# Performance work log

Measured on AMD Instinct MI355X. Metric: run time of the kernel, lower is better.

Reference implementation:

```python
import jax, jax.numpy as jnp
import numpy as np

B, S, HID, H = 1, 2048, 512, 8
D = HID // H            # head_dim = 64
N_TIP, N_FAC = 16, 256
SCALE = 1.0 / np.sqrt(D).astype(np.float32)


def _dominant_dim_indices():
    # dominant_fcs = arange(n_tip) % (head_dim//2), identical for every head
    pair_dim = max(1, D // 2)
    fc = jnp.arange(N_TIP) % pair_dim                      # [n_tip]
    dim_idx = jnp.stack((fc * 2, fc * 2 + 1), axis=-1).reshape(-1)  # [2*n_tip]
    return jnp.clip(dim_idx, 0, D - 1)


def setup_inputs() -> dict:
    key = jax.random.key(0)
    kx, kq, kk, kv, ko = jax.random.split(key, 5)
    s = 1.0 / np.sqrt(HID)
    return {
        "x": jax.random.normal(kx, (B, S, HID), jnp.float32),
        "wq": jax.random.normal(kq, (HID, HID), jnp.float32) * s,
        "wk": jax.random.normal(kk, (HID, HID), jnp.float32) * s,
        "wv": jax.random.normal(kv, (HID, HID), jnp.float32) * s,
        "wo": jax.random.normal(ko, (HID, HID), jnp.float32) * s,
    }


def reference(x, wq, wk, wv, wo):
    # projections (nn.Linear, no bias): y = x @ W.T; split into heads -> [B,H,S,D]
    def split_heads(y):
        return y.reshape(B, S, H, D).transpose(0, 2, 1, 3)

    q = split_heads(x @ wq.T)
    k = split_heads(x @ wk.T)
    v = split_heads(x @ wv.T)

    dim_idx = _dominant_dim_indices()                      # [2*n_tip]
    q_sub = q[..., dim_idx]                                # [B,H,S,2*n_tip]
    k_sub = k[..., dim_idx]
    importance = jnp.einsum("bhqf,bhkf->bhqk", q_sub, k_sub)  # [B,H,S,S]

    n_sel = min(N_FAC, S)
    _, top_idx = jax.lax.top_k(importance, n_sel)          # [B,H,S,n_sel]

    # gather selected K/V per query: [B,H,S,n_sel,D]
    k_sel = jnp.take_along_axis(k[:, :, None], top_idx[..., None], axis=3)
    v_sel = jnp.take_along_axis(v[:, :, None], top_idx[..., None], axis=3)

    scores = jnp.einsum("bhqd,bhqkd->bhqk", q, k_sel) * SCALE
    attn = jax.nn.softmax(scores, axis=-1)
    out = jnp.einsum("bhqk,bhqkd->bhqd", attn, v_sel)      # [B,H,S,D]

    out = out.transpose(0, 2, 1, 3).reshape(B, S, HID)
    return out @ wo.T
```

## Files before the change

### kernel.cpp

```cpp
#include <hip/hip_runtime.h>

#define S_LEN  2048
#define HIDDEN 512
#define NHEAD  8
#define DHEAD  64
#define NSEL   256
#define ROWS_A 8
#define SCALE_ 0.125f

#define WAVE_SYNC() __asm__ volatile("s_waitcnt lgkmcnt(0)" ::: "memory")

__device__ __forceinline__ unsigned mapu(float f) {
  unsigned u = __float_as_uint(f);
  return (u & 0x80000000u) ? ~u : (u | 0x80000000u);
}
__device__ __forceinline__ float unmapu(unsigned x) {
  return __uint_as_float((x & 0x80000000u) ? (x & 0x7FFFFFFFu) : ~x);
}

union H4 { _Float16 h[4]; uint2 u2; };

__device__ __forceinline__ void gemm_nt_body(const float* __restrict__ A,
                                             const float* __restrict__ B,
                                             float* __restrict__ C,
                                             int K, int N, int m0, int n0,
                                             float (*As)[68], float (*Bs)[68]) {
  const int t  = threadIdx.x;
  const int tx = t & 15, ty = t >> 4;
  const int rr = t >> 3, cc = (t & 7) << 2;
  float acc[4][4] = {};

  float4 fa0 = *(const float4*)&A[(size_t)(m0 + rr)      * K + cc];
  float4 fa1 = *(const float4*)&A[(size_t)(m0 + rr + 32) * K + cc];
  float4 fb0 = *(const float4*)&B[(size_t)(n0 + rr)      * K + cc];
  float4 fb1 = *(const float4*)&B[(size_t)(n0 + rr + 32) * K + cc];

  for (int k0 = 0; k0 < K; k0 += 32) {
    __syncthreads();
    As[cc + 0][rr] = fa0.x; As[cc + 1][rr] = fa0.y; As[cc + 2][rr] = fa0.z; As[cc + 3][rr] = fa0.w;
    As[cc + 0][rr + 32] = fa1.x; As[cc + 1][rr + 32] = fa1.y; As[cc + 2][rr + 32] = fa1.z; As[cc + 3][rr + 32] = fa1.w;
    Bs[cc + 0][rr] = fb0.x; Bs[cc + 1][rr] = fb0.y; Bs[cc + 2][rr] = fb0.z; Bs[cc + 3][rr] = fb0.w;
    Bs[cc + 0][rr + 32] = fb1.x; Bs[cc + 1][rr + 32] = fb1.y; Bs[cc + 2][rr + 32] = fb1.z; Bs[cc + 3][rr + 32] = fb1.w;
    __syncthreads();
    if (k0 + 32 < K) {
      fa0 = *(const float4*)&A[(size_t)(m0 + rr)      * K + k0 + 32 + cc];
      fa1 = *(const float4*)&A[(size_t)(m0 + rr + 32) * K + k0 + 32 + cc];
      fb0 = *(const float4*)&B[(size_t)(n0 + rr)      * K + k0 + 32 + cc];
      fb1 = *(const float4*)&B[(size_t)(n0 + rr + 32) * K + k0 + 32 + cc];
    }
#pragma unroll
    for (int kk = 0; kk < 32; ++kk) {
      const float4 a4 = *(const float4*)&As[kk][ty * 4];
      const float4 b4 = *(const float4*)&Bs[kk][tx * 4];
      const float a[4] = {a4.x, a4.y, a4.z, a4.w};
      const float b[4] = {b4.x, b4.y, b4.z, b4.w};
#pragma unroll
      for (int i = 0; i < 4; ++i)
#pragma unroll
        for (int j = 0; j < 4; ++j) acc[i][j] += a[i] * b[j];
    }
  }
#pragma unroll
  for (int i = 0; i < 4; ++i) {
    float4 o = make_float4(acc[i][0], acc[i][1], acc[i][2], acc[i][3]);
    *(float4*)&C[(size_t)(m0 + ty * 4 + i) * N + n0 + tx * 4] = o;
  }
}

__global__ __launch_bounds__(256) void gemm_nt(const float* __restrict__ A,
                                               const float* __restrict__ B,
                                               float* __restrict__ C,
                                               int M, int N, int K) {
  __shared__ float As[32][68];
  __shared__ float Bs[32][68];
  gemm_nt_body(A, B, C, K, N, blockIdx.x * 64, blockIdx.y * 64, As, Bs);
}

__global__ __launch_bounds__(256) void gemm_qkv(const float* __restrict__ x,
                                                const float* __restrict__ wq,
                                                const float* __restrict__ wk,
                                                const float* __restrict__ wv,
                                                float* __restrict__ Qb,
                                                float* __restrict__ Kb,
                                                float* __restrict__ Vb) {
  __shared__ float As[32][68];
  __shared__ float Bs[32][68];
  const int z = blockIdx.z;
  const float* B = (z == 0) ? wq : (z == 1) ? wk : wv;
  float*       C = (z == 0) ? Qb : (z == 1) ? Kb : Vb;
  gemm_nt_body(x, B, C, HIDDEN, HIDDEN, blockIdx.x * 64, blockIdx.y * 64, As, Bs);
}

__global__ __launch_bounds__(256) void score_gemm(const float* __restrict__ Q,
                                                  const float* __restrict__ K,
                                                  unsigned* __restrict__ impu,
                                                  _Float16* __restrict__ sch) {
  __shared__ float Qs[64][132];
  __shared__ float Ks[64][68];
  const int bid  = blockIdx.x;
  const int h    = bid & (NHEAD - 1);
  const int tile = bid >> 3;
  const int q0   = (tile & 15) * 128;
  const int k0   = (tile >> 4) * 64;
  const int t  = threadIdx.x;
  const int tx = t & 15, ty = t >> 4;

#pragma unroll
  for (int s = 0; s < 8; ++s) {
    const int sf = s * 256 + t;
    const int r = sf >> 4, c = (sf & 15) * 4;
    const float4 f = *(const float4*)&Q[(size_t)(q0 + r) * HIDDEN + h * DHEAD + c];
    Qs[c + 0][r] = f.x; Qs[c + 1][r] = f.y; Qs[c + 2][r] = f.z; Qs[c + 3][r] = f.w;
  }
#pragma unroll
  for (int s = 0; s < 4; ++s) {
    const int sf = s * 256 + t;
    const int r = sf >> 4, c = (sf & 15) * 4;
    const float4 f = *(const float4*)&K[(size_t)(k0 + r) * HIDDEN + h * DHEAD + c];
    Ks[c + 0][r] = f.x; Ks[c + 1][r] = f.y; Ks[c + 2][r] = f.z; Ks[c + 3][r] = f.w;
  }
  __syncthreads();

  float acc[8][4] = {};
#pragma unroll
  for (int d = 0; d < 32; ++d) {
    const float4 aa = *(const float4*)&Qs[d][ty * 8];
    const float4 ab = *(const float4*)&Qs[d][ty * 8 + 4];
    const float4 b4 = *(const float4*)&Ks[d][tx * 4];
    const float a[8] = {aa.x, aa.y, aa.z, aa.w, ab.x, ab.y, ab.z, ab.w};
    const float b[4] = {b4.x, b4.y, b4.z, b4.w};
#pragma unroll
    for (int i = 0; i < 8; ++i)
#pragma unroll
      for (int j = 0; j < 4; ++j) acc[i][j] += a[i] * b[j];
  }
  float simp[8][4];
#pragma unroll
  for (int i = 0; i < 8; ++i)
#pragma unroll
    for (int j = 0; j < 4; ++j) simp[i][j] = acc[i][j];
#pragma unroll
  for (int d = 32; d < 64; ++d) {
    const float4 aa = *(const float4*)&Qs[d][ty * 8];
    const float4 ab = *(const float4*)&Qs[d][ty * 8 + 4];
    const float4 b4 = *(const float4*)&Ks[d][tx * 4];
    const float a[8] = {aa.x, aa.y, aa.z, aa.w, ab.x, ab.y, ab.z, ab.w};
    const float b[4] = {b4.x, b4.y, b4.z, b4.w};
#pragma unroll
    for (int i = 0; i < 8; ++i)
#pragma unroll
      for (int j = 0; j < 4; ++j) acc[i][j] += a[i] * b[j];
  }

#pragma unroll
  for (int i = 0; i < 8; ++i) {
    const size_t gr = (size_t)(h * S_LEN) + q0 + ty * 8 + i;
    const size_t off = gr * S_LEN + k0 + tx * 4;
    *(uint4*)&impu[off] = make_uint4(mapu(simp[i][0]), mapu(simp[i][1]),
                                     mapu(simp[i][2]), mapu(simp[i][3]));
    H4 pk;
#pragma unroll
    for (int j = 0; j < 4; ++j) pk.h[j] = (_Float16)(acc[i][j] * SCALE_);
    *(uint2*)&sch[off] = pk.u2;
  }
}

__global__ __launch_bounds__(512) void fused_select_pv(const unsigned* __restrict__ impu,
                                                       const _Float16* __restrict__ sch,
                                                       const float* __restrict__ V,
                                                       float* __restrict__ AO) {
  __shared__ unsigned hist[ROWS_A][256];
  __shared__ float    sbuf[ROWS_A][NSEL];
  __shared__ unsigned ibuf[ROWS_A][NSEL];
  __shared__ unsigned short eqbuf[ROWS_A][64];
  __shared__ unsigned rstate[ROWS_A][2];

  const int t = threadIdx.x, wv = t >> 6, lane = t & 63;
  const unsigned long long lmask = (1ull << lane) - 1ull;
  const size_t gr = (size_t)blockIdx.x * ROWS_A + wv;
  const unsigned* rowp  = impu + gr * S_LEN;
  const _Float16* shrow = sch  + gr * S_LEN;

  uint4 u[8];
  H4    s4[8];
#pragma unroll
  for (int j = 0; j < 8; ++j) {
    u[j]     = *(const uint4*)&rowp[j * 256 + lane * 4];
    s4[j].u2 = *(const uint2*)&shrow[j * 256 + lane * 4];
  }

  unsigned um = u[0].x, uM = u[0].x;
#pragma unroll
  for (int j = 0; j < 8; ++j) {
    um = min(um, min(min(u[j].x, u[j].y), min(u[j].z, u[j].w)));
    uM = max(uM, max(max(u[j].x, u[j].y), max(u[j].z, u[j].w)));
  }
#pragma unroll
  for (int off = 32; off; off >>= 1) {
    um = min(um, (unsigned)__shfl_xor((int)um, off));
    uM = max(uM, (unsigned)__shfl_xor((int)uM, off));
  }

  unsigned bn[8];
  unsigned T;
  if (uM == um) {
    T = uM;
  } else {
    const float vmin  = unmapu(um);
    const float scale = 255.0f / (unmapu(uM) - vmin);

    *(uint4*)&hist[wv][lane * 4] = make_uint4(0u, 0u, 0u, 0u);
    WAVE_SYNC();
#pragma unroll
    for (int j = 0; j < 8; ++j) {
      const unsigned uu[4] = {u[j].x, u[j].y, u[j].z, u[j].w};
      unsigned pk = 0;
#pragma unroll
      for (int e = 0; e < 4; ++e) {
        int bb = (int)((unmapu(uu[e]) - vmin) * scale);
        bb = bb < 0 ? 0 : (bb > 255 ? 255 : bb);
        pk |= (unsigned)bb << (8 * e);
        atomicAdd(&hist[wv][bb], 1u);
      }
      bn[j] = pk;
    }
    WAVE_SYNC();
    {
      const int g = 63 - lane;
      const uint4 c4 = *(const uint4*)&hist[wv][4 * g];
      const unsigned c0 = c4.x, c1 = c4.y, c2 = c4.z, c3 = c4.w;
      const unsigned lsum = c0 + c1 + c2 + c3;
      unsigned incl = lsum;
#pragma unroll
      for (int off = 1; off < 64; off <<= 1) {
        unsigned o = __shfl_up(incl, off);
        if (lane >= off) incl += o;
      }
      const unsigned excl = incl - lsum;
      const unsigned ab3 = excl, ab2 = excl + c3, ab1 = excl + c3 + c2, ab0 = excl + c3 + c2 + c1;
      if (ab3 < NSEL && NSEL <= ab3 + c3) { rstate[wv][0] = 4u*g+3u; rstate[wv][1] = NSEL - ab3; }
      if (ab2 < NSEL && NSEL <= ab2 + c2) { rstate[wv][0] = 4u*g+2u; rstate[wv][1] = NSEL - ab2; }
      if (ab1 < NSEL && NSEL <= ab1 + c1) { rstate[wv][0] = 4u*g+1u; rstate[wv][1] = NSEL - ab1; }
      if (ab0 < NSEL && NSEL <= ab0 + c0) { rstate[wv][0] = 4u*g+0u; rstate[wv][1] = NSEL - ab0; }
    }
    WAVE_SYNC();
    const unsigned B    = rstate[wv][0];
    const unsigned krem = rstate[wv][1];
    const unsigned nb   = hist[wv][B];

    if (nb <= 64) {
      unsigned* ebufu = (unsigned*)&sbuf[wv][0];
      unsigned nbase = 0;
#pragma unroll
      for (int j = 0; j < 8; ++j) {
        const unsigned uu[4] = {u[j].x, u[j].y, u[j].z, u[j].w};
#pragma unroll
        for (int e = 0; e < 4; ++e) {
          const bool inb = (((bn[j] >> (8 * e)) & 0xFFu) == B);
          const unsigned long long m = __ballot(inb);
          if (inb) ebufu[nbase + (unsigned)__popcll(m & lmask)] = uu[e];
          nbase += (unsigned)__popcll(m);
        }
      }
      WAVE_SYNC();
      const unsigned myv = (lane < (int)nb) ? ebufu[lane] : 0u;
      unsigned gtc = 0, eqc = 0;
      for (unsigned jj = 0; jj < nb; ++jj) {
        const unsigned bv = (unsigned)__shfl((int)myv, (int)jj);
        gtc += (bv > myv) ? 1u : 0u;
        eqc += (bv == myv) ? 1u : 0u;
      }
      if (lane < (int)nb && gtc < krem && krem <= gtc + eqc) rstate[wv][0] = myv;
      WAVE_SYNC();
      T = rstate[wv][0];
    } else {
      unsigned m2min = 0xFFFFFFFFu, m2max = 0u;
      for (int i = lane; i < S_LEN; i += 64) {
        const unsigned x = rowp[i];
        int bb = (int)((unmapu(x) - vmin) * scale);
        bb = bb < 0 ? 0 : (bb > 255 ? 255 : bb);
        if (bb == (int)B) { m2min = min(m2min, x); m2max = max(m2max, x); }
      }
#pragma unroll
      for (int off = 32; off; off >>= 1) {
        m2min = min(m2min, (unsigned)__shfl_xor((int)m2min, off));
        m2max = max(m2max, (unsigned)__shfl_xor((int)m2max, off));
      }
      if (m2max == m2min) {
        T = m2max;
      } else {
        const float vlo2   = unmapu(m2min);
        const float scale2 = 255.0f / (unmapu(m2max) - vlo2);
        *(uint4*)&hist[wv][lane * 4] = make_uint4(0u, 0u, 0u, 0u);
        WAVE_SYNC();
        for (int i = lane; i < S_LEN; i += 64) {
          const unsigned x = rowp[i];
          const float v = unmapu(x);
          int bb = (int)((v - vmin) * scale);
          bb = bb < 0 ? 0 : (bb > 255 ? 255 : bb);
          if (bb == (int)B) {
            int b2 = (int)((v - vlo2) * scale2);
            b2 = b2 < 0 ? 0 : (b2 > 255 ? 255 : b2);
            atomicAdd(&hist[wv][b2], 1u);
          }
        }
        WAVE_SYNC();
        {
          const int g = 63 - lane;
          const uint4 c4 = *(const uint4*)&hist[wv][4 * g];
          const unsigned c0 = c4.x, c1 = c4.y, c2 = c4.z, c3 = c4.w;
          const unsigned lsum = c0 + c1 + c2 + c3;
          unsigned incl = lsum;
#pragma unroll
          for (int off = 1; off < 64; off <<= 1) {
            unsigned o = __shfl_up(incl, off);
            if (lane >= off) incl += o;
          }
          const unsigned excl = incl - lsum;
          const unsigned ab3 = excl, ab2 = excl + c3, ab1 = excl + c3 + c2, ab0 = excl + c3 + c2 + c1;
          if (ab3 < krem && krem <= ab3 + c3) { rstate[wv][0] = 4u*g+3u; rstate[wv][1] = krem - ab3; }
          if (ab2 < krem && krem <= ab2 + c2) { rstate[wv][0] = 4u*g+2u; rstate[wv][1] = krem - ab2; }
          if (ab1 < krem && krem <= ab1 + c1) { rstate[wv][0] = 4u*g+1u; rstate[wv][1] = krem - ab1; }
          if (ab0 < krem && krem <= ab0 + c0) { rstate[wv][0] = 4u*g+0u; rstate[wv][1] = krem - ab0; }
        }
        WAVE_SYNC();
        const unsigned B2    = rstate[wv][0];
        const unsigned krem2 = rstate[wv][1];
        const unsigned nb2   = hist[wv][B2];
        if (nb2 <= 64) {
          unsigned* ebufu = (unsigned*)&sbuf[wv][0];
          unsigned nbase = 0;
          for (int i = lane; i < S_LEN; i += 64) {
            const unsigned x = rowp[i];
            const float v = unmapu(x);
            int bb = (int)((v - vmin) * scale);
            bb = bb < 0 ? 0 : (bb > 255 ? 255 : bb);
            bool inb = false;
            if (bb == (int)B) {
              int b2 = (int)((v - vlo2) * scale2);
              b2 = b2 < 0 ? 0 : (b2 > 255 ? 255 : b2);
              inb = (b2 == (int)B2);
            }
            const unsigned long long m = __ballot(inb);
            if (inb) ebufu[nbase + (unsigned)__popcll(m & lmask)] = x;
            nbase += (unsigned)__popcll(m);
          }
          WAVE_SYNC();
          const unsigned myv = (lane < (int)nb2) ? ebufu[lane] : 0u;
          unsigned gtc = 0, eqc = 0;
          for (unsigned jj = 0; jj < nb2; ++jj) {
            const unsigned bv = (unsigned)__shfl((int)myv, (int)jj);
            gtc += (bv > myv) ? 1u : 0u;
            eqc += (bv == myv) ? 1u : 0u;
          }
          if (lane < (int)nb2 && gtc < krem2 && krem2 <= gtc + eqc) rstate[wv][0] = myv;
          WAVE_SYNC();
          T = rstate[wv][0];
        } else {
          if (lane == 0) {
            unsigned pfx = 0, kr = NSEL;
            for (int rb = 3; rb >= 0; --rb) {
              for (int i2 = 0; i2 < 256; ++i2) hist[wv][i2] = 0u;
              for (int i2 = 0; i2 < S_LEN; ++i2) {
                const unsigned x = rowp[i2];
                if (rb == 3 || ((x >> (rb * 8 + 8)) == pfx)) hist[wv][(x >> (rb * 8)) & 0xFF]++;
              }
              unsigned cum = 0, sel = 0;
              for (int bb2 = 255; bb2 >= 0; --bb2) {
                if (kr <= cum + hist[wv][bb2]) { sel = (unsigned)bb2; kr -= cum; break; }
                cum += hist[wv][bb2];
              }
              pfx = (pfx << 8) | sel;
            }
            rstate[wv][0] = pfx;
          }
          WAVE_SYNC();
          T = rstate[wv][0];
        }
      }
    }
  }

  unsigned base_gt = 0, base_eq = 0;
#pragma unroll
  for (int j = 0; j < 8; ++j) {
    const unsigned uu[4] = {u[j].x, u[j].y, u[j].z, u[j].w};
#pragma unroll
    for (int e = 0; e < 4; ++e) {
      const unsigned v = uu[e];
      const int i = j * 256 + lane * 4 + e;
      const bool gt = (v > T), eq = (v == T);
      const unsigned long long mg = __ballot(gt);
      const unsigned long long me = __ballot(eq);
      if (gt) {
        const unsigned p = base_gt + (unsigned)__popcll(mg & lmask);
        ibuf[wv][p] = (unsigned)i << 9;
        sbuf[wv][p] = (float)s4[j].h[e];
      }
      if (eq) {
        const unsigned p = base_eq + (unsigned)__popcll(me & lmask);
        if (p < 64) eqbuf[wv][p] = (unsigned short)i;
      }
      base_gt += (unsigned)__popcll(mg);
      base_eq += (unsigned)__popcll(me);
    }
  }
  WAVE_SYNC();
  const unsigned ngt = base_gt, ne = base_eq;
  const unsigned need = NSEL - ngt;
  if (ne == need && ne <= 64) {
    for (unsigned j = lane; j < ne; j += 64) {
      const unsigned short ix = eqbuf[wv][j];
      ibuf[wv][ngt + j] = (unsigned)ix << 9;
      sbuf[wv][ngt + j] = (float)shrow[ix];
    }
  } else if (lane == 0) {
    if (ne <= 64) {
      for (unsigned j = 0; j < need; ++j) {
        const unsigned short ix = eqbuf[wv][j];
        ibuf[wv][ngt + j] = (unsigned)ix << 9;
        sbuf[wv][ngt + j] = (float)shrow[ix];
      }
    } else {
      unsigned taken = 0;
      for (int i = 0; i < S_LEN && taken < need; ++i)
        if (rowp[i] == T) { ibuf[wv][ngt + taken] = (unsigned)i << 9; sbuf[wv][ngt + taken] = (float)shrow[i]; ++taken; }
    }
  }
  WAVE_SYNC();

  float sc[4];
#pragma unroll
  for (int m = 0; m < 4; ++m) sc[m] = sbuf[wv][lane * 4 + m];
  float mx = fmaxf(fmaxf(sc[0], sc[1]), fmaxf(sc[2], sc[3]));
#pragma unroll
  for (int off = 32; off; off >>= 1) mx = fmaxf(mx, __shfl_xor(mx, off));
  float zs = 0.f;
#pragma unroll
  for (int m = 0; m < 4; ++m) { sc[m] = expf(sc[m] - mx); zs += sc[m]; }
#pragma unroll
  for (int off = 32; off; off >>= 1) zs += __shfl_xor(zs, off);
  const float rz = 1.0f / zs;
  *(float4*)&sbuf[wv][lane * 4] = make_float4(sc[0], sc[1], sc[2], sc[3]);
  WAVE_SYNC();

  const int h = (int)(gr >> 11), q = (int)(gr & (S_LEN - 1));
  const float* Vhl = V + h * DHEAD + lane;
  float outv = 0.f;
#pragma unroll 8
  for (int j = 0; j < NSEL; j += 4) {
    const uint4  id4 = *(const uint4*)&ibuf[wv][j];
    const float4 w4  = *(const float4*)&sbuf[wv][j];
    outv += w4.x * Vhl[id4.x];
    outv += w4.y * Vhl[id4.y];
    outv += w4.z * Vhl[id4.z];
    outv += w4.w * Vhl[id4.w];
  }
  AO[(size_t)q * HIDDEN + h * DHEAD + lane] = outv * rz;
}

extern "C" void kernel_launch(void* const* d_in, const int* in_sizes, int n_in,
                              void* d_out, int out_size, void* d_ws, size_t ws_size,
                              hipStream_t stream) {
  const float* x  = (const float*)d_in[0];
  const float* wq = (const float*)d_in[1];
  const float* wk = (const float*)d_in[2];
  const float* wv = (const float*)d_in[3];
  const float* wo = (const float*)d_in[4];
  float* out = (float*)d_out;

  float* Qb = (float*)d_ws;
  float* Kb = Qb + (size_t)S_LEN * HIDDEN;
  float* Vb = Kb + (size_t)S_LEN * HIDDEN;
  float* AO = Vb + (size_t)S_LEN * HIDDEN;
  void*  tail = (void*)(AO + (size_t)S_LEN * HIDDEN);

  const size_t elems = (size_t)NHEAD * S_LEN * S_LEN;
  unsigned* impu = (unsigned*)tail;
  _Float16* sch  = (_Float16*)(impu + elems);

  dim3 g(S_LEN / 64, HIDDEN / 64);
  gemm_qkv<<<dim3(S_LEN / 64, HIDDEN / 64, 3), 256, 0, stream>>>(x, wq, wk, wv, Qb, Kb, Vb);
  score_gemm<<<dim3(NHEAD * 16 * 32), 256, 0, stream>>>(Qb, Kb, impu, sch);
  fused_select_pv<<<dim3(NHEAD * S_LEN / ROWS_A), 512, 0, stream>>>(impu, sch, Vb, AO);
  gemm_nt<<<g, 256, 0, stream>>>(AO, wo, out, S_LEN, HIDDEN, HIDDEN);
}
```

Measured before the change: 224.1 us.

## Split-K output GEMM with atomics and bucket-ordered top-k scatter

Replaces the final output projection with a split-K=2 GEMM that accumulates into a zeroed output through float atomics, doubling the block count for the small GEMM. In the selection kernel, the sequential ballot/popcount compaction of elements above the threshold is replaced with a scatter driven by per-bucket histogram prefix offsets and LDS atomics. Tie elements are sorted by index afterwards so the selection stays deterministic. The costs are an extra memset, atomic write traffic, and nondeterministic float summation order in the output.

```diff
diff --git a/kernel.cpp b/kernel.cpp
--- a/kernel.cpp
+++ b/kernel.cpp
@@ -65,15 +65,6 @@
     float4 o = make_float4(acc[i][0], acc[i][1], acc[i][2], acc[i][3]);
     *(float4*)&C[(size_t)(m0 + ty * 4 + i) * N + n0 + tx * 4] = o;
   }
-}
-
-__global__ __launch_bounds__(256) void gemm_nt(const float* __restrict__ A,
-                                               const float* __restrict__ B,
-                                               float* __restrict__ C,
-                                               int M, int N, int K) {
-  __shared__ float As[32][68];
-  __shared__ float Bs[32][68];
-  gemm_nt_body(A, B, C, K, N, blockIdx.x * 64, blockIdx.y * 64, As, Bs);
 }
 
 __global__ __launch_bounds__(256) void gemm_qkv(const float* __restrict__ x,
@@ -91,6 +82,56 @@
   gemm_nt_body(x, B, C, HIDDEN, HIDDEN, blockIdx.x * 64, blockIdx.y * 64, As, Bs);
 }
 
+__global__ __launch_bounds__(256) void gemm_nt_sk2(const float* __restrict__ A,
+                                                   const float* __restrict__ B,
+                                                   float* __restrict__ C,
+                                                   int M, int N, int K) {
+  __shared__ float As[32][68];
+  __shared__ float Bs[32][68];
+  const int m0 = blockIdx.x * 64, n0 = blockIdx.y * 64;
+  const int kb0 = blockIdx.z * (K / 2), kb1 = kb0 + K / 2;
+  const int t  = threadIdx.x;
+  const int tx = t & 15, ty = t >> 4;
+  const int rr = t >> 3, cc = (t & 7) << 2;
+  float acc[4][4] = {};
+
+  float4 fa0 = *(const float4*)&A[(size_t)(m0 + rr)      * K + kb0 + cc];
+  float4 fa1 = *(const float4*)&A[(size_t)(m0 + rr + 32) * K + kb0 + cc];
+  float4 fb0 = *(const float4*)&B[(size_t)(n0 + rr)      * K + kb0 + cc];
+  float4 fb1 = *(const float4*)&B[(size_t)(n0 + rr + 32) * K + kb0 + cc];
+
+  for (int k0 = kb0; k0 < kb1; k0 += 32) {
+    __syncthreads();
+    As[cc + 0][rr] = fa0.x; As[cc + 1][rr] = fa0.y; As[cc + 2][rr] = fa0.z; As[cc + 3][rr] = fa0.w;
+    As[cc + 0][rr + 32] = fa1.x; As[cc + 1][rr + 32] = fa1.y; As[cc + 2][rr + 32] = fa1.z; As[cc + 3][rr + 32] = fa1.w;
+    Bs[cc + 0][rr] = fb0.x; Bs[cc + 1][rr] = fb0.y; Bs[cc + 2][rr] = fb0.z; Bs[cc + 3][rr] = fb0.w;
+    Bs[cc + 0][rr + 32] = fb1.x; Bs[cc + 1][rr + 32] = fb1.y; Bs[cc + 2][rr + 32] = fb1.z; Bs[cc + 3][rr + 32] = fb1.w;
+    __syncthreads();
+    if (k0 + 32 < kb1) {
+      fa0 = *(const float4*)&A[(size_t)(m0 + rr)      * K + k0 + 32 + cc];
+      fa1 = *(const float4*)&A[(size_t)(m0 + rr + 32) * K + k0 + 32 + cc];
+      fb0 = *(const float4*)&B[(size_t)(n0 + rr)      * K + k0 + 32 + cc];
+      fb1 = *(const float4*)&B[(size_t)(n0 + rr + 32) * K + k0 + 32 + cc];
+    }
+#pragma unroll
+    for (int kk = 0; kk < 32; ++kk) {
+      const float4 a4 = *(const float4*)&As[kk][ty * 4];
+      const float4 b4 = *(const float4*)&Bs[kk][tx * 4];
+      const float a[4] = {a4.x, a4.y, a4.z, a4.w};
+      const float b[4] = {b4.x, b4.y, b4.z, b4.w};
+#pragma unroll
+      for (int i = 0; i < 4; ++i)
+#pragma unroll
+        for (int j = 0; j < 4; ++j) acc[i][j] += a[i] * b[j];
+    }
+  }
+#pragma unroll
+  for (int i = 0; i < 4; ++i)
+#pragma unroll
+    for (int j = 0; j < 4; ++j)
+      atomicAdd(&C[(size_t)(m0 + ty * 4 + i) * N + n0 + tx * 4 + j], acc[i][j]);
+}
+
 __global__ __launch_bounds__(256) void score_gemm(const float* __restrict__ Q,
                                                   const float* __restrict__ K,
                                                   unsigned* __restrict__ impu,
@@ -170,10 +211,12 @@
                                                        const float* __restrict__ V,
                                                        float* __restrict__ AO) {
   __shared__ unsigned hist[ROWS_A][256];
+  __shared__ unsigned offs[ROWS_A][256];
   __shared__ float    sbuf[ROWS_A][NSEL];
   __shared__ unsigned ibuf[ROWS_A][NSEL];
   __shared__ unsigned short eqbuf[ROWS_A][64];
   __shared__ unsigned rstate[ROWS_A][2];
+  __shared__ unsigned cntEq[ROWS_A];
 
   const int t = threadIdx.x, wv = t >> 6, lane = t & 63;
   const unsigned long long lmask = (1ull << lane) - 1ull;
@@ -202,9 +245,13 @@
   }
 
   unsigned bn[8];
-  unsigned T;
+  unsigned T, Bsel;
   if (uM == um) {
-    T = uM;
+    T = uM; Bsel = 0;
+#pragma unroll
+    for (int j = 0; j < 8; ++j) bn[j] = 0u;
+    if (lane == 0) offs[wv][0] = 0u;
+    WAVE_SYNC();
   } else {
     const float vmin  = unmapu(um);
     const float scale = 255.0f / (unmapu(uM) - vmin);
@@ -237,6 +284,10 @@
         if (lane >= off) incl += o;
       }
       const unsigned excl = incl - lsum;
+      offs[wv][4*g+3] = excl;
+      offs[wv][4*g+2] = excl + c3;
+      offs[wv][4*g+1] = excl + c3 + c2;
+      offs[wv][4*g+0] = excl + c3 + c2 + c1;
       const unsigned ab3 = excl, ab2 = excl + c3, ab1 = excl + c3 + c2, ab0 = excl + c3 + c2 + c1;
       if (ab3 < NSEL && NSEL <= ab3 + c3) { rstate[wv][0] = 4u*g+3u; rstate[wv][1] = NSEL - ab3; }
       if (ab2 < NSEL && NSEL <= ab2 + c2) { rstate[wv][0] = 4u*g+2u; rstate[wv][1] = NSEL - ab2; }
@@ -247,6 +298,7 @@
     const unsigned B    = rstate[wv][0];
     const unsigned krem = rstate[wv][1];
     const unsigned nb   = hist[wv][B];
+    Bsel = B;
 
     if (nb <= 64) {
       unsigned* ebufu = (unsigned*)&sbuf[wv][0];
@@ -274,10 +326,11 @@
       WAVE_SYNC();
       T = rstate[wv][0];
     } else {
+      const float vmin1 = vmin; const float scale1 = scale;
       unsigned m2min = 0xFFFFFFFFu, m2max = 0u;
       for (int i = lane; i < S_LEN; i += 64) {
         const unsigned x = rowp[i];
-        int bb = (int)((unmapu(x) - vmin) * scale);
+        int bb = (int)((unmapu(x) - vmin1) * scale1);
         bb = bb < 0 ? 0 : (bb > 255 ? 255 : bb);
         if (bb == (int)B) { m2min = min(m2min, x); m2max = max(m2max, x); }
       }
@@ -296,7 +349,7 @@
         for (int i = lane; i < S_LEN; i += 64) {
           const unsigned x = rowp[i];
           const float v = unmapu(x);
-          int bb = (int)((v - vmin) * scale);
+          int bb = (int)((v - vmin1) * scale1);
           bb = bb < 0 ? 0 : (bb > 255 ? 255 : bb);
           if (bb == (int)B) {
             int b2 = (int)((v - vlo2) * scale2);
@@ -333,7 +386,7 @@
           for (int i = lane; i < S_LEN; i += 64) {
             const unsigned x = rowp[i];
             const float v = unmapu(x);
-            int bb = (int)((v - vmin) * scale);
+            int bb = (int)((v - vmin1) * scale1);
             bb = bb < 0 ? 0 : (bb > 255 ? 255 : bb);
             bool inb = false;
             if (bb == (int)B) {
@@ -381,7 +434,8 @@
     }
   }
 
-  unsigned base_gt = 0, base_eq = 0;
+  if (lane == 0) cntEq[wv] = 0;
+  WAVE_SYNC();
 #pragma unroll
   for (int j = 0; j < 8; ++j) {
     const unsigned uu[4] = {u[j].x, u[j].y, u[j].z, u[j].w};
@@ -389,24 +443,26 @@
     for (int e = 0; e < 4; ++e) {
       const unsigned v = uu[e];
       const int i = j * 256 + lane * 4 + e;
-      const bool gt = (v > T), eq = (v == T);
-      const unsigned long long mg = __ballot(gt);
-      const unsigned long long me = __ballot(eq);
-      if (gt) {
-        const unsigned p = base_gt + (unsigned)__popcll(mg & lmask);
+      const unsigned b = (bn[j] >> (8 * e)) & 0xFFu;
+      if (b > Bsel) {
+        const unsigned p = atomicAdd(&offs[wv][b], 1u);
         ibuf[wv][p] = (unsigned)i << 9;
         sbuf[wv][p] = (float)s4[j].h[e];
-      }
-      if (eq) {
-        const unsigned p = base_eq + (unsigned)__popcll(me & lmask);
-        if (p < 64) eqbuf[wv][p] = (unsigned short)i;
-      }
-      base_gt += (unsigned)__popcll(mg);
-      base_eq += (unsigned)__popcll(me);
+      } else if (b == Bsel) {
+        if (v > T) {
+          const unsigned p = atomicAdd(&offs[wv][Bsel], 1u);
+          ibuf[wv][p] = (unsigned)i << 9;
+          sbuf[wv][p] = (float)s4[j].h[e];
+        } else if (v == T) {
+          const unsigned p = atomicAdd(&cntEq[wv], 1u);
+          if (p < 64) eqbuf[wv][p] = (unsigned short)i;
+        }
+      }
     }
   }
   WAVE_SYNC();
-  const unsigned ngt = base_gt, ne = base_eq;
+  const unsigned ngt = offs[wv][Bsel];
+  const unsigned ne  = cntEq[wv];
   const unsigned need = NSEL - ngt;
   if (ne == need && ne <= 64) {
     for (unsigned j = lane; j < ne; j += 64) {
@@ -416,6 +472,11 @@
     }
   } else if (lane == 0) {
     if (ne <= 64) {
+      for (unsigned a = 1; a < ne; ++a) {
+        unsigned short kv = eqbuf[wv][a]; int bp = (int)a;
+        while (bp > 0 && eqbuf[wv][bp - 1] > kv) { eqbuf[wv][bp] = eqbuf[wv][bp - 1]; --bp; }
+        eqbuf[wv][bp] = kv;
+      }
       for (unsigned j = 0; j < need; ++j) {
         const unsigned short ix = eqbuf[wv][j];
         ibuf[wv][ngt + j] = (unsigned)ix << 9;
@@ -479,9 +540,9 @@
   unsigned* impu = (unsigned*)tail;
   _Float16* sch  = (_Float16*)(impu + elems);
 
-  dim3 g(S_LEN / 64, HIDDEN / 64);
   gemm_qkv<<<dim3(S_LEN / 64, HIDDEN / 64, 3), 256, 0, stream>>>(x, wq, wk, wv, Qb, Kb, Vb);
   score_gemm<<<dim3(NHEAD * 16 * 32), 256, 0, stream>>>(Qb, Kb, impu, sch);
   fused_select_pv<<<dim3(NHEAD * S_LEN / ROWS_A), 512, 0, stream>>>(impu, sch, Vb, AO);
-  gemm_nt<<<g, 256, 0, stream>>>(AO, wo, out, S_LEN, HIDDEN, HIDDEN);
-}
+  hipMemsetAsync(out, 0, (size_t)S_LEN * HIDDEN * sizeof(float), stream);
+  gemm_nt_sk2<<<dim3(S_LEN / 64, HIDDEN / 64, 2), 256, 0, stream>>>(AO, wo, out, S_LEN, HIDDEN, HIDDEN);
+}
```

Result: slower. 280.4 us (+25.1%).
